# Optimization experiments

Hardware: AMD Instinct MI355X
Metric: run time of the kernel (lower is better)

## Reference

```python
import jax, jax.numpy as jnp
import numpy as np

H = 16          # num_heads
EPS = 1e-6      # RMSNorm eps


def setup_inputs() -> dict:
    key = jax.random.key(0)
    ks = jax.random.split(key, 5)
    B, N, D = 4, 4096, 1024
    x = jax.random.normal(ks[0], (B, N, D), dtype=jnp.float32)
    q = jax.random.normal(ks[1], (D,), dtype=jnp.float32)
    k = jax.random.normal(ks[2], (D,), dtype=jnp.float32)
    log_decay = jax.random.normal(ks[3], (H,), dtype=jnp.float32)
    norm_weight = jnp.ones((D,), dtype=jnp.float32)
    o_w = jax.random.normal(ks[4], (D, D), dtype=jnp.float32) * 0.02
    return {"x": x, "q": q, "k": k, "log_decay": log_decay,
            "norm_weight": norm_weight, "o_w": o_w}


def reference(x, q, k, log_decay, norm_weight, o_w):
    b, n, dm = x.shape
    dh = dm // H
    qh = q.reshape(H, dh)            # per-head query vector (constant over b, n)
    kh = k.reshape(H, dh)            # per-head key vector
    v = x.reshape(b, n, H, dh)       # values = input tokens
    # exp(logsigmoid(a)) == sigmoid(a): per-head decay in (0, 1)
    lam = jax.nn.sigmoid(log_decay)  # (H,)

    def step(S, v_t):
        # S: (b, H, dh, dh) recurrent state;  v_t: (b, H, dh)
        S = lam[None, :, None, None] * S + kh[None, :, :, None] * v_t[:, :, None, :]
        o_t = jnp.einsum('hd,bhdv->bhv', qh, S)
        return S, o_t

    S0 = jnp.zeros((b, H, dh, dh), dtype=x.dtype)
    _, o = jax.lax.scan(step, S0, jnp.moveaxis(v, 1, 0))  # o: (n, b, H, dh)
    o = jnp.moveaxis(o, 0, 1).reshape(b, n, dm)

    # RMSNorm over the channel dim
    o = o * jax.lax.rsqrt(jnp.mean(o * o, axis=-1, keepdims=True) + EPS) * norm_weight
    # o_proj (no bias)
    return o @ o_w.T
```

## Files before the change

### kernel.cpp

```cpp
#include <hip/hip_runtime.h>
#include <hip/hip_bf16.h>
#include <cstdint>
#include <cstddef>

#define HH   16
#define BB   4
#define NN   4096
#define DD   1024
#define MM   (BB * NN)
#define NC   128
#define LC   32
#define EPSV 1e-6f

typedef short short8 __attribute__((ext_vector_type(8)));
typedef float floatx4 __attribute__((ext_vector_type(4)));

__device__ __forceinline__ void async_copy16(const void* g, void* l) {
    __builtin_amdgcn_global_load_lds(
        (const __attribute__((address_space(1))) void*)g,
        (__attribute__((address_space(3))) void*)l, 16, 0, 0);
}

__global__ void k_meta(const float* __restrict__ q, const float* __restrict__ k,
                       const float* __restrict__ ld, float* __restrict__ meta) {
    int tid = threadIdx.x;
    float p = q[tid] * k[tid];
    #pragma unroll
    for (int off = 32; off > 0; off >>= 1) p += __shfl_xor(p, off);
    if ((tid & 63) == 0) meta[16 + (tid >> 6)] = p;
    if (tid < HH) meta[tid] = 1.f / (1.f + expf(-ld[tid]));
}

__global__ void k_wconv(const float* __restrict__ ow, const float* __restrict__ nw,
                        __hip_bfloat16* __restrict__ wp) {
    size_t i = (size_t)blockIdx.x * 256 + threadIdx.x;
    int j = (int)(i & (DD - 1));
    wp[i] = __float2bfloat16(ow[i] * nw[j]);
}

__global__ void k_chunk_end(const float* __restrict__ x, const float* __restrict__ meta,
                            float* __restrict__ E) {
    int b = blockIdx.x >> 7, c = blockIdx.x & (NC - 1);
    int j = threadIdx.x;
    float lam = meta[j >> 6];
    const float* xp = x + ((size_t)(b * NN + c * LC)) * DD + j;
    float e = 0.f;
    #pragma unroll
    for (int t = 0; t < LC; ++t) e = fmaf(lam, e, xp[(size_t)t * DD]);
    E[(size_t)blockIdx.x * DD + j] = e;
}

__global__ void k_carry(const float* __restrict__ meta, const float* __restrict__ E,
                        float* __restrict__ P) {
    __shared__ float sa[NC], sb[NC];
    int chain = blockIdx.x;
    int b = chain >> 10, j = chain & 1023;
    int c = threadIdx.x;
    float lam = meta[j >> 6];
    float lamL = lam;
    lamL *= lamL; lamL *= lamL; lamL *= lamL; lamL *= lamL; lamL *= lamL;
    size_t idx = ((size_t)(b * NC + c)) * DD + j;
    float a = lamL, bv = E[idx];
    sa[c] = a; sb[c] = bv;
    #pragma unroll
    for (int d = 1; d < NC; d <<= 1) {
        __syncthreads();
        float pa = 1.f, pb = 0.f;
        if (c >= d) { pa = sa[c - d]; pb = sb[c - d]; }
        __syncthreads();
        bv = fmaf(a, pb, bv);
        a  = a * pa;
        sa[c] = a; sb[c] = bv;
    }
    __syncthreads();
    P[idx] = (c == 0) ? 0.f : sb[c - 1];
}

__global__ void k_scan(const float* __restrict__ x, const float* __restrict__ meta,
                       const float* __restrict__ P, __hip_bfloat16* __restrict__ obf,
                       float* __restrict__ sumsq) {
    int b = blockIdx.x >> 7, c = blockIdx.x & (NC - 1);
    int j = threadIdx.x;
    int h = j >> 6;
    float lam = meta[h];
    float ch  = meta[16 + h];
    int row0 = b * NN + c * LC;
    const float* xp = x + (size_t)row0 * DD + j;
    float y = P[(size_t)blockIdx.x * DD + j];
    for (int t = 0; t < LC; ++t) {
        y = fmaf(lam, y, xp[(size_t)t * DD]);
        float o = ch * y;
        obf[(size_t)(row0 + t) * DD + j] = __float2bfloat16(o);
        float s = o * o;
        #pragma unroll
        for (int off = 32; off > 0; off >>= 1) s += __shfl_xor(s, off);
        if ((j & 63) == 0) atomicAdd(&sumsq[row0 + t], s);
    }
}

__launch_bounds__(256)
__global__ void k_gemm(const __hip_bfloat16* __restrict__ A,
                       const __hip_bfloat16* __restrict__ W,
                       const float* __restrict__ sumsq, float* __restrict__ out) {
    __shared__ __attribute__((aligned(16))) short sA[128 * 64];
    __shared__ __attribute__((aligned(16))) short sB[128 * 64];
    const int tid = threadIdx.x;
    const int l = tid & 63, w = tid >> 6;
    const int wm = w >> 1, wn = w & 1;
    const int g = blockIdx.x;
    const int bm = g & 127, bn = g >> 7;
    const int m0 = bm * 128, n0 = bn * 128;
    const short* Ag = (const short*)A;
    const short* Wg = (const short*)W;

    floatx4 acc[4][4] = {};

    int srow[4], scol[4];
    #pragma unroll
    for (int i = 0; i < 4; ++i) {
        int s = i * 256 + tid;
        srow[i] = s >> 3;
        scol[i] = ((s & 7) ^ ((s >> 3) & 7)) * 8;
    }

    for (int kt = 0; kt < 16; ++kt) {
        const int k0 = kt * 64;
        #pragma unroll
        for (int i = 0; i < 4; ++i) {
            async_copy16(Ag + (size_t)(m0 + srow[i]) * 1024 + k0 + scol[i],
                         (char*)sA + i * 4096 + w * 1024);
            async_copy16(Wg + (size_t)(n0 + srow[i]) * 1024 + k0 + scol[i],
                         (char*)sB + i * 4096 + w * 1024);
        }
        __syncthreads();
        #pragma unroll
        for (int ks = 0; ks < 2; ++ks) {
            short8 af[4], bf[4];
            #pragma unroll
            for (int mt = 0; mt < 4; ++mt) {
                int row = wm * 64 + mt * 16 + (l & 15);
                int c8  = (ks * 4 + (l >> 4)) ^ (row & 7);
                af[mt] = *(const short8*)(sA + row * 64 + c8 * 8);
            }
            #pragma unroll
            for (int nt = 0; nt < 4; ++nt) {
                int row = wn * 64 + nt * 16 + (l & 15);
                int c8  = (ks * 4 + (l >> 4)) ^ (row & 7);
                bf[nt] = *(const short8*)(sB + row * 64 + c8 * 8);
            }
            #pragma unroll
            for (int mt = 0; mt < 4; ++mt)
                #pragma unroll
                for (int nt = 0; nt < 4; ++nt)
                    acc[mt][nt] = __builtin_amdgcn_mfma_f32_16x16x32_bf16(af[mt], bf[nt], acc[mt][nt], 0, 0, 0);
        }
        __syncthreads();
    }

    #pragma unroll
    for (int mt = 0; mt < 4; ++mt) {
        #pragma unroll
        for (int r = 0; r < 4; ++r) {
            int mrow = m0 + wm * 64 + mt * 16 + (l >> 4) * 4 + r;
            float rs = rsqrtf(sumsq[mrow] * (1.f / 1024.f) + EPSV);
            #pragma unroll
            for (int nt = 0; nt < 4; ++nt) {
                int col = n0 + wn * 64 + nt * 16 + (l & 15);
                out[(size_t)mrow * 1024 + col] = acc[mt][nt][r] * rs;
            }
        }
    }
}

extern "C" void kernel_launch(void* const* d_in, const int* in_sizes, int n_in,
                              void* d_out, int out_size, void* d_ws, size_t ws_size,
                              hipStream_t stream) {
    const float* x  = (const float*)d_in[0];
    const float* q  = (const float*)d_in[1];
    const float* k  = (const float*)d_in[2];
    const float* ld = (const float*)d_in[3];
    const float* nw = (const float*)d_in[4];
    const float* ow = (const float*)d_in[5];
    float* out = (float*)d_out;

    char* ws = (char*)d_ws;
    float* meta  = (float*)(ws + 0);
    float* sumsq = (float*)(ws + 256);
    float* E     = (float*)(ws + 65792);
    float* P     = (float*)(ws + 2162944);
    __hip_bfloat16* Wp  = (__hip_bfloat16*)(ws + 4260096);
    __hip_bfloat16* Obf = (__hip_bfloat16*)(ws + 6357248);

    hipMemsetAsync(sumsq, 0, MM * sizeof(float), stream);
    k_meta<<<1, 1024, 0, stream>>>(q, k, ld, meta);
    k_wconv<<<(DD * DD) / 256, 256, 0, stream>>>(ow, nw, Wp);
    k_chunk_end<<<BB * NC, 1024, 0, stream>>>(x, meta, E);
    k_carry<<<BB * DD, NC, 0, stream>>>(meta, E, P);
    k_scan<<<BB * NC, 1024, 0, stream>>>(x, meta, P, Obf, sumsq);
    k_gemm<<<(MM / 128) * (DD / 128), 256, 0, stream>>>(Obf, Wp, sumsq, out);
}
```

Measured before the change: 199.9 us.

## Vectorize scan kernels with float4 and make carry a tiled serial scan

```diff
diff --git a/kernel.cpp b/kernel.cpp
--- a/kernel.cpp
+++ b/kernel.cpp
@@ -21,6 +21,13 @@
         (__attribute__((address_space(3))) void*)l, 16, 0, 0);
 }
 
+__device__ __forceinline__ uint2 pack_bf16x4(float a, float b, float c, float d) {
+    union { __hip_bfloat16 h[4]; uint2 u; } cv;
+    cv.h[0] = __float2bfloat16(a); cv.h[1] = __float2bfloat16(b);
+    cv.h[2] = __float2bfloat16(c); cv.h[3] = __float2bfloat16(d);
+    return cv.u;
+}
+
 __global__ void k_meta(const float* __restrict__ q, const float* __restrict__ k,
                        const float* __restrict__ ld, float* __restrict__ meta) {
     int tid = threadIdx.x;
@@ -33,68 +40,83 @@
 
 __global__ void k_wconv(const float* __restrict__ ow, const float* __restrict__ nw,
                         __hip_bfloat16* __restrict__ wp) {
-    size_t i = (size_t)blockIdx.x * 256 + threadIdx.x;
-    int j = (int)(i & (DD - 1));
-    wp[i] = __float2bfloat16(ow[i] * nw[j]);
+    size_t i4 = (size_t)blockIdx.x * 256 + threadIdx.x;
+    int j = (int)((i4 * 4) & (DD - 1));
+    float4 v = ((const float4*)ow)[i4];
+    ((uint2*)wp)[i4] = pack_bf16x4(v.x * nw[j], v.y * nw[j + 1],
+                                   v.z * nw[j + 2], v.w * nw[j + 3]);
 }
 
 __global__ void k_chunk_end(const float* __restrict__ x, const float* __restrict__ meta,
                             float* __restrict__ E) {
     int b = blockIdx.x >> 7, c = blockIdx.x & (NC - 1);
-    int j = threadIdx.x;
-    float lam = meta[j >> 6];
-    const float* xp = x + ((size_t)(b * NN + c * LC)) * DD + j;
-    float e = 0.f;
-    #pragma unroll
-    for (int t = 0; t < LC; ++t) e = fmaf(lam, e, xp[(size_t)t * DD]);
-    E[(size_t)blockIdx.x * DD + j] = e;
+    int j4 = threadIdx.x;
+    float lam = meta[(j4 * 4) >> 6];
+    const float4* xp = (const float4*)(x + ((size_t)(b * NN + c * LC)) * DD) + j4;
+    float4 e = {0.f, 0.f, 0.f, 0.f};
+    #pragma unroll
+    for (int t = 0; t < LC; ++t) {
+        float4 v = xp[(size_t)t * (DD / 4)];
+        e.x = fmaf(lam, e.x, v.x); e.y = fmaf(lam, e.y, v.y);
+        e.z = fmaf(lam, e.z, v.z); e.w = fmaf(lam, e.w, v.w);
+    }
+    ((float4*)(E + (size_t)blockIdx.x * DD))[j4] = e;
 }
 
 __global__ void k_carry(const float* __restrict__ meta, const float* __restrict__ E,
                         float* __restrict__ P) {
-    __shared__ float sa[NC], sb[NC];
-    int chain = blockIdx.x;
-    int b = chain >> 10, j = chain & 1023;
-    int c = threadIdx.x;
-    float lam = meta[j >> 6];
-    float lamL = lam;
-    lamL *= lamL; lamL *= lamL; lamL *= lamL; lamL *= lamL; lamL *= lamL;
-    size_t idx = ((size_t)(b * NC + c)) * DD + j;
-    float a = lamL, bv = E[idx];
-    sa[c] = a; sb[c] = bv;
-    #pragma unroll
-    for (int d = 1; d < NC; d <<= 1) {
-        __syncthreads();
-        float pa = 1.f, pb = 0.f;
-        if (c >= d) { pa = sa[c - d]; pb = sb[c - d]; }
-        __syncthreads();
-        bv = fmaf(a, pb, bv);
-        a  = a * pa;
-        sa[c] = a; sb[c] = bv;
+    __shared__ float tile[NC][33];
+    int b = blockIdx.x >> 5, jg = blockIdx.x & 31;
+    int tid = threadIdx.x;
+    int cc = tid >> 5, jj = tid & 31;
+    #pragma unroll
+    for (int it = 0; it < 16; ++it) {
+        int c = it * 8 + cc;
+        tile[c][jj] = E[(size_t)(b * NC + c) * DD + jg * 32 + jj];
     }
     __syncthreads();
-    P[idx] = (c == 0) ? 0.f : sb[c - 1];
+    if (tid < 32) {
+        int j = jg * 32 + tid;
+        float lam = meta[j >> 6];
+        float lamL = lam;
+        lamL *= lamL; lamL *= lamL; lamL *= lamL; lamL *= lamL; lamL *= lamL;
+        float p = 0.f;
+        for (int c = 0; c < NC; ++c) {
+            float e = tile[c][tid];
+            tile[c][tid] = p;
+            p = fmaf(lamL, p, e);
+        }
+    }
+    __syncthreads();
+    #pragma unroll
+    for (int it = 0; it < 16; ++it) {
+        int c = it * 8 + cc;
+        P[(size_t)(b * NC + c) * DD + jg * 32 + jj] = tile[c][jj];
+    }
 }
 
 __global__ void k_scan(const float* __restrict__ x, const float* __restrict__ meta,
                        const float* __restrict__ P, __hip_bfloat16* __restrict__ obf,
                        float* __restrict__ sumsq) {
     int b = blockIdx.x >> 7, c = blockIdx.x & (NC - 1);
-    int j = threadIdx.x;
-    int h = j >> 6;
+    int j4 = threadIdx.x;
+    int h = (j4 * 4) >> 6;
     float lam = meta[h];
     float ch  = meta[16 + h];
     int row0 = b * NN + c * LC;
-    const float* xp = x + (size_t)row0 * DD + j;
-    float y = P[(size_t)blockIdx.x * DD + j];
+    const float4* xp = (const float4*)(x + (size_t)row0 * DD) + j4;
+    float4 y = ((const float4*)(P + (size_t)blockIdx.x * DD))[j4];
+    int lane0 = ((threadIdx.x & 63) == 0);
     for (int t = 0; t < LC; ++t) {
-        y = fmaf(lam, y, xp[(size_t)t * DD]);
-        float o = ch * y;
-        obf[(size_t)(row0 + t) * DD + j] = __float2bfloat16(o);
-        float s = o * o;
+        float4 v = xp[(size_t)t * (DD / 4)];
+        y.x = fmaf(lam, y.x, v.x); y.y = fmaf(lam, y.y, v.y);
+        y.z = fmaf(lam, y.z, v.z); y.w = fmaf(lam, y.w, v.w);
+        float ox = ch * y.x, oy = ch * y.y, oz = ch * y.z, ow = ch * y.w;
+        ((uint2*)(obf + (size_t)(row0 + t) * DD))[j4] = pack_bf16x4(ox, oy, oz, ow);
+        float s = ox * ox + oy * oy + oz * oz + ow * ow;
         #pragma unroll
         for (int off = 32; off > 0; off >>= 1) s += __shfl_xor(s, off);
-        if ((j & 63) == 0) atomicAdd(&sumsq[row0 + t], s);
+        if (lane0) atomicAdd(&sumsq[row0 + t], s);
     }
 }
 
@@ -193,9 +215,9 @@
 
     hipMemsetAsync(sumsq, 0, MM * sizeof(float), stream);
     k_meta<<<1, 1024, 0, stream>>>(q, k, ld, meta);
-    k_wconv<<<(DD * DD) / 256, 256, 0, stream>>>(ow, nw, Wp);
-    k_chunk_end<<<BB * NC, 1024, 0, stream>>>(x, meta, E);
-    k_carry<<<BB * DD, NC, 0, stream>>>(meta, E, P);
-    k_scan<<<BB * NC, 1024, 0, stream>>>(x, meta, P, Obf, sumsq);
+    k_wconv<<<(DD * DD / 4) / 256, 256, 0, stream>>>(ow, nw, Wp);
+    k_chunk_end<<<BB * NC, 256, 0, stream>>>(x, meta, E);
+    k_carry<<<BB * 32, 256, 0, stream>>>(meta, E, P);
+    k_scan<<<BB * NC, 256, 0, stream>>>(x, meta, P, Obf, sumsq);
     k_gemm<<<(MM / 128) * (DD / 128), 256, 0, stream>>>(Obf, Wp, sumsq, out);
 }
```

Result: faster. 190.2 us (-4.9%).
